# Kernel tuning notes

Hardware: AMD Instinct MI355X
Metric: run time of the kernel (lower is better)

The kernel has to match this reference:

```python
import jax, jax.numpy as jnp
import numpy as np

D_MODEL = 1024
N_HEADS = 16
D_KEY = 64
EPS = 1e-5


def setup_inputs() -> dict:
    key = jax.random.key(0)
    ks = jax.random.split(key, 12)
    d, h, dk = D_MODEL, N_HEADS, D_KEY
    s = lambda fan_in: 1.0 / np.sqrt(fan_in)
    inp = {
        "X": jax.random.normal(ks[0], (2, 2048, d), dtype=jnp.float32),
        "Wqkv": jax.random.uniform(ks[1], (d, 3 * h * dk), jnp.float32, -s(d), s(d)),
        "bqkv": jax.random.uniform(ks[2], (3 * h * dk,), jnp.float32, -s(d), s(d)),
        "Wo": jax.random.uniform(ks[3], (h * dk, d), jnp.float32, -s(h * dk), s(h * dk)),
        "bo": jax.random.uniform(ks[4], (d,), jnp.float32, -s(h * dk), s(h * dk)),
        "W1": jax.random.uniform(ks[5], (d, 4 * d), jnp.float32, -s(d), s(d)),
        "b1": jax.random.uniform(ks[6], (4 * d,), jnp.float32, -s(d), s(d)),
        "W2": jax.random.uniform(ks[7], (4 * d, d), jnp.float32, -s(4 * d), s(4 * d)),
        "b2": jax.random.uniform(ks[8], (d,), jnp.float32, -s(4 * d), s(4 * d)),
        "ln1_g": jnp.ones((d,), jnp.float32),
        "ln1_b": jnp.zeros((d,), jnp.float32),
        "ln2_g": jnp.ones((d,), jnp.float32),
        "ln2_b": jnp.zeros((d,), jnp.float32),
    }
    return inp


def _layernorm(x, g, b):
    mu = jnp.mean(x, axis=-1, keepdims=True)
    var = jnp.var(x, axis=-1, keepdims=True)
    return (x - mu) * jax.lax.rsqrt(var + EPS) * g + b


def _block(X, Wqkv, bqkv, Wo, bo, W1, b1, W2, b2, ln1_g, ln1_b, ln2_g, ln2_b):
    B, T, _ = X.shape
    h, dk = N_HEADS, D_KEY
    # --- causal multi-head self-attention on LN(X) ---
    Xn = _layernorm(X, ln1_g, ln1_b)
    qkv = (Xn @ Wqkv + bqkv).reshape(B, T, 3, h, dk)
    q, k, v = (jnp.moveaxis(qkv, 2, 0)[i].transpose(0, 2, 1, 3) for i in range(3))  # each [B,h,T,dk]
    scores = jnp.einsum("bhqd,bhkd->bhqk", q, k) / np.sqrt(dk).astype(np.float32)
    causal = jnp.tril(jnp.ones((T, T), dtype=bool))
    scores = jnp.where(causal, scores, -jnp.inf)
    attn = jax.nn.softmax(scores, axis=-1)
    ctx = jnp.einsum("bhqk,bhkd->bhqd", attn, v)  # [B,h,T,dk]
    ctx = ctx.transpose(0, 2, 1, 3).reshape(B, T, h * dk)
    atten = ctx @ Wo + bo
    X = X + atten  # dropout is identity in eval mode
    # --- FFN on LN(X) ---
    Xn2 = _layernorm(X, ln2_g, ln2_b)
    ffn = jax.nn.relu(Xn2 @ W1 + b1) @ W2 + b2
    return X + ffn


def reference(X, Wqkv, bqkv, Wo, bo, W1, b1, W2, b2, ln1_g, ln1_b, ln2_g, ln2_b):
    return _block(X, Wqkv, bqkv, Wo, bo, W1, b1, W2, b2, ln1_g, ln1_b, ln2_g, ln2_b)
```

## Files before the change

kernel.cpp:

```cpp
#include <hip/hip_runtime.h>
#include <hip/hip_bf16.h>

typedef __hip_bfloat16 bf16;
typedef __attribute__((ext_vector_type(8))) short short8;
typedef __attribute__((ext_vector_type(4))) float f32x4;

constexpr int D     = 1024;
constexpr int T     = 2048;
constexpr int BATCH = 2;
constexpr int ROWS  = BATCH * T;
constexpr int NH    = 16;
constexpr int DKEY  = 64;
constexpr int QKVN  = 3 * D;
constexpr int FFNN  = 4 * D;

static __device__ __forceinline__ float b2f(bf16 x) { return __bfloat162float(x); }
static __device__ __forceinline__ bf16  f2b(float x) { return __float2bfloat16(x); }
static __device__ __forceinline__ float loadf(const bf16* p)  { return __bfloat162float(*p); }
static __device__ __forceinline__ float loadf(const float* p) { return *p; }
static __device__ __forceinline__ float fast_exp2(float x) { return __builtin_amdgcn_exp2f(x); }
static __device__ __forceinline__ unsigned short f2bu(float x) {
    return __bfloat16_as_ushort(__float2bfloat16(x));
}

__global__ __launch_bounds__(256) void transpose_cast(const float* __restrict__ in,
                                                      bf16* __restrict__ out,
                                                      int R, int C)
{
    __shared__ float tile[32][33];
    int c0 = blockIdx.x * 32, r0 = blockIdx.y * 32;
    int tx = threadIdx.x & 31, ty = threadIdx.x >> 5;
#pragma unroll
    for (int i = 0; i < 32; i += 8)
        tile[ty + i][tx] = in[(size_t)(r0 + ty + i) * C + c0 + tx];
    __syncthreads();
#pragma unroll
    for (int i = 0; i < 32; i += 8)
        out[(size_t)(c0 + ty + i) * R + r0 + tx] = f2b(tile[tx][ty + i]);
}

template <typename TIN>
__global__ __launch_bounds__(256) void ln_kernel(const TIN* __restrict__ X,
                                                 const float* __restrict__ g,
                                                 const float* __restrict__ b,
                                                 bf16* __restrict__ out)
{
    int row = blockIdx.x;
    int tid = threadIdx.x;
    const TIN* xr = X + (size_t)row * D;
    float v[4];
#pragma unroll
    for (int i = 0; i < 4; ++i) v[i] = loadf(xr + tid + i * 256);

    float s1 = v[0] + v[1] + v[2] + v[3];
    float s2 = v[0]*v[0] + v[1]*v[1] + v[2]*v[2] + v[3]*v[3];
#pragma unroll
    for (int off = 32; off; off >>= 1) {
        s1 += __shfl_xor(s1, off);
        s2 += __shfl_xor(s2, off);
    }
    __shared__ float red[8];
    int lane = tid & 63, w = tid >> 6;
    if (lane == 0) { red[w] = s1; red[4 + w] = s2; }
    __syncthreads();
    s1 = red[0] + red[1] + red[2] + red[3];
    s2 = red[4] + red[5] + red[6] + red[7];

    float mu   = s1 * (1.0f / D);
    float var  = s2 * (1.0f / D) - mu * mu;
    float rstd = rsqrtf(var + 1e-5f);

    bf16* orow = out + (size_t)row * D;
#pragma unroll
    for (int i = 0; i < 4; ++i) {
        int c = tid + i * 256;
        orow[c] = f2b((v[i] - mu) * rstd * g[c] + b[c]);
    }
}

template <int BM, int RELU, int RES, int OUTF32>
__global__ __launch_bounds__(256) void mfma_gemm(
    const bf16* __restrict__ A, const bf16* __restrict__ Bt,
    const float* __restrict__ bias, const void* __restrict__ resid,
    void* __restrict__ out, int M, int N, int K)
{
    constexpr int LDSK = 40;
    constexpr int MT   = BM / 32;
    __shared__ __align__(16) unsigned short As[2][BM * LDSK];
    __shared__ __align__(16) unsigned short Bs[2][128 * LDSK];

    int tid  = threadIdx.x;
    int m0   = blockIdx.y * BM, n0 = blockIdx.x * 128;
    int lane = tid & 63, wave = tid >> 6;
    int wm = (wave >> 1) * (MT * 16), wn = (wave & 1) * 64;
    int c15 = lane & 15, quad = lane >> 4;

    f32x4 acc[MT][4] = {};

    int brow = tid >> 1, bseg = (tid & 1) * 16;
    int arow, aseg;
    if constexpr (BM == 128) { arow = tid >> 1; aseg = (tid & 1) * 16; }
    else                     { arow = tid >> 2; aseg = (tid & 3) * 8;  }
    const bf16* aptr = A  + (size_t)(m0 + arow) * K + aseg;
    const bf16* bptr = Bt + (size_t)(n0 + brow) * K + bseg;

    int nk = K >> 5;
    uint4 ra0, ra1, rb0, rb1;
    ra0 = *(const uint4*)(aptr);
    if constexpr (BM == 128) ra1 = *(const uint4*)(aptr + 8);
    rb0 = *(const uint4*)(bptr);
    rb1 = *(const uint4*)(bptr + 8);

    for (int kt = 0; kt < nk; ++kt) {
        int buf = kt & 1;
        {
            unsigned short* asl = &As[buf][arow * LDSK + aseg];
            unsigned short* bsl = &Bs[buf][brow * LDSK + bseg];
            *(uint4*)asl = ra0;
            if constexpr (BM == 128) *(uint4*)(asl + 8) = ra1;
            *(uint4*)bsl       = rb0;
            *(uint4*)(bsl + 8) = rb1;
        }
        __syncthreads();
        if (kt + 1 < nk) {
            int ko = (kt + 1) * 32;
            ra0 = *(const uint4*)(aptr + ko);
            if constexpr (BM == 128) ra1 = *(const uint4*)(aptr + ko + 8);
            rb0 = *(const uint4*)(bptr + ko);
            rb1 = *(const uint4*)(bptr + ko + 8);
        }
        short8 af[MT], bfr[4];
#pragma unroll
        for (int t = 0; t < MT; ++t)
            af[t]  = *(const short8*)&As[buf][(wm + t * 16 + c15) * LDSK + quad * 8];
#pragma unroll
        for (int t = 0; t < 4; ++t)
            bfr[t] = *(const short8*)&Bs[buf][(wn + t * 16 + c15) * LDSK + quad * 8];
#pragma unroll
        for (int mt = 0; mt < MT; ++mt)
#pragma unroll
            for (int nt = 0; nt < 4; ++nt)
                acc[mt][nt] = __builtin_amdgcn_mfma_f32_16x16x32_bf16(
                    af[mt], bfr[nt], acc[mt][nt], 0, 0, 0);
    }

#pragma unroll
    for (int mt = 0; mt < MT; ++mt) {
#pragma unroll
        for (int nt = 0; nt < 4; ++nt) {
            f32x4 v4 = acc[mt][nt];
            int gc = n0 + wn + nt * 16 + c15;
            float bb = bias[gc];
#pragma unroll
            for (int r = 0; r < 4; ++r) {
                int gr = m0 + wm + mt * 16 + quad * 4 + r;
                float v = v4[r] + bb;
                if constexpr (RELU) v = fmaxf(v, 0.0f);
                size_t idx = (size_t)gr * N + gc;
                if constexpr (RES == 1) v += b2f(((const bf16*)resid)[idx]);
                if constexpr (RES == 2) v += ((const float*)resid)[idx];
                if constexpr (OUTF32) ((float*)out)[idx] = v;
                else                  ((bf16*)out)[idx] = f2b(v);
            }
        }
    }
}

__global__ __launch_bounds__(256) void flash_attn(const bf16* __restrict__ qkv,
                                                  bf16* __restrict__ ctx)
{
    constexpr int KROW = 72;
    constexpr float CSC = 0.18033688011112042f;
    constexpr float MSH = 12.0f;

    __shared__ __align__(16) unsigned short Qs[128 * KROW];
    __shared__ __align__(16) unsigned short Ks[64 * KROW];
    __shared__ __align__(16) unsigned short Vt[64 * KROW];
    unsigned short* Pt = Qs;

    int bx = blockIdx.x;
    int bh = bx & 31;
    int qi = 15 - (bx >> 5);
    int h  = bh & 15, b = bh >> 4;
    int q0 = qi * 128;

    int tid = threadIdx.x, lane = tid & 63, w = tid >> 6;
    int c15 = lane & 15, quad = lane >> 4;

    const bf16* base = qkv + (size_t)b * T * QKVN;

    {
        int row = tid >> 1, half = tid & 1;
        const bf16* src = base + (size_t)(q0 + row) * QKVN + h * 64 + half * 32;
        unsigned short* dst = &Qs[row * KROW + half * 32];
        uint4 v0 = *(const uint4*)(src);
        uint4 v1 = *(const uint4*)(src + 8);
        uint4 v2 = *(const uint4*)(src + 16);
        uint4 v3 = *(const uint4*)(src + 24);
        *(uint4*)(dst)      = v0;
        *(uint4*)(dst + 8)  = v1;
        *(uint4*)(dst + 16) = v2;
        *(uint4*)(dst + 24) = v3;
    }
    __syncthreads();

    short8 qf[2][2];
#pragma unroll
    for (int qt = 0; qt < 2; ++qt)
#pragma unroll
        for (int s = 0; s < 2; ++s)
            qf[qt][s] = *(const short8*)&Qs[(w * 32 + qt * 16 + c15) * KROW + s * 32 + quad * 8];

    short8 ones;
#pragma unroll
    for (int i = 0; i < 8; ++i) ones[i] = (short)0x3F80;

    f32x4 Ot[4][2] = {};
    f32x4 lacc[2]  = {};

    int nkt   = q0 / 64 + 2;
    int wqmin = q0 + w * 32;
    int wqmax = wqmin + 31;

    for (int kt = 0; kt < nkt; ++kt) {
        int k0 = kt * 64;
        int key = tid >> 2, seg = tid & 3;
        const bf16* ksrc = base + (size_t)(k0 + key) * QKVN + D + h * 64 + seg * 16;
        uint4 kv0 = *(const uint4*)ksrc;
        uint4 kv1 = *(const uint4*)(ksrc + 8);
        int keyp = (tid & 31) * 2, dk0 = (tid >> 5) * 8;
        const bf16* vsrc = base + (size_t)(k0 + keyp) * QKVN + 2 * D + h * 64 + dk0;
        uint4 vv0 = *(const uint4*)vsrc;
        uint4 vv1 = *(const uint4*)(vsrc + QKVN);

        __syncthreads();
        {
            unsigned short* kd = &Ks[key * KROW + seg * 16];
            *(uint4*)kd       = kv0;
            *(uint4*)(kd + 8) = kv1;
            const unsigned short* lo = (const unsigned short*)&vv0;
            const unsigned short* hi = (const unsigned short*)&vv1;
#pragma unroll
            for (int j = 0; j < 8; ++j) {
                unsigned int pk = (unsigned int)lo[j] | ((unsigned int)hi[j] << 16);
                *(unsigned int*)&Vt[(dk0 + j) * KROW + keyp] = pk;
            }
        }
        __syncthreads();

        if (k0 <= wqmax) {
            f32x4 St[4][2] = {};
#pragma unroll
            for (int s = 0; s < 2; ++s)
#pragma unroll
                for (int ktm = 0; ktm < 4; ++ktm) {
                    short8 kf = *(const short8*)&Ks[(ktm * 16 + c15) * KROW + s * 32 + quad * 8];
#pragma unroll
                    for (int qt = 0; qt < 2; ++qt)
                        St[ktm][qt] = __builtin_amdgcn_mfma_f32_16x16x32_bf16(
                            kf, qf[qt][s], St[ktm][qt], 0, 0, 0);
                }

            bool diag = (k0 + 63 > wqmin);
#pragma unroll
            for (int ktm = 0; ktm < 4; ++ktm)
#pragma unroll
                for (int qt = 0; qt < 2; ++qt) {
                    ushort4 pk;
                    int q_g = wqmin + qt * 16 + c15;
#pragma unroll
                    for (int r = 0; r < 4; ++r) {
                        float p = fast_exp2(fmaf(St[ktm][qt][r], CSC, -MSH));
                        if (diag && (k0 + ktm * 16 + quad * 4 + r > q_g)) p = 0.0f;
                        ((unsigned short*)&pk)[r] = f2bu(p);
                    }
                    *(ushort4*)&Pt[(w * 32 + qt * 16 + c15) * KROW + ktm * 16 + quad * 4] = pk;
                }

#pragma unroll
            for (int s = 0; s < 2; ++s) {
                short8 pf[2];
#pragma unroll
                for (int qt = 0; qt < 2; ++qt)
                    pf[qt] = *(const short8*)&Pt[(w * 32 + qt * 16 + c15) * KROW + s * 32 + quad * 8];
#pragma unroll
                for (int qt = 0; qt < 2; ++qt)
                    lacc[qt] = __builtin_amdgcn_mfma_f32_16x16x32_bf16(ones, pf[qt], lacc[qt], 0, 0, 0);
#pragma unroll
                for (int dt = 0; dt < 4; ++dt) {
                    short8 vf = *(const short8*)&Vt[(dt * 16 + c15) * KROW + s * 32 + quad * 8];
#pragma unroll
                    for (int qt = 0; qt < 2; ++qt)
                        Ot[dt][qt] = __builtin_amdgcn_mfma_f32_16x16x32_bf16(
                            vf, pf[qt], Ot[dt][qt], 0, 0, 0);
                }
            }
        }
    }

#pragma unroll
    for (int qt = 0; qt < 2; ++qt) {
        float inv = 1.0f / lacc[qt][0];
        int grow = b * T + q0 + w * 32 + qt * 16 + c15;
        bf16* dst = ctx + (size_t)grow * D + h * 64 + quad * 4;
#pragma unroll
        for (int dt = 0; dt < 4; ++dt) {
            ushort4 pk;
#pragma unroll
            for (int r = 0; r < 4; ++r)
                ((unsigned short*)&pk)[r] = f2bu(Ot[dt][qt][r] * inv);
            *(ushort4*)(dst + dt * 16) = pk;
        }
    }
}

extern "C" void kernel_launch(void* const* d_in, const int* in_sizes, int n_in,
                              void* d_out, int out_size, void* d_ws, size_t ws_size,
                              hipStream_t stream)
{
    const float* X    = (const float*)d_in[0];
    const float* Wqkv = (const float*)d_in[1];
    const float* bqkv = (const float*)d_in[2];
    const float* Wo   = (const float*)d_in[3];
    const float* bo   = (const float*)d_in[4];
    const float* W1   = (const float*)d_in[5];
    const float* b1   = (const float*)d_in[6];
    const float* W2   = (const float*)d_in[7];
    const float* b2   = (const float*)d_in[8];
    const float* ln1g = (const float*)d_in[9];
    const float* ln1b = (const float*)d_in[10];
    const float* ln2g = (const float*)d_in[11];
    const float* ln2b = (const float*)d_in[12];
    float* out = (float*)d_out;

    char* ws = (char*)d_ws;
    bf16* Wqkv_t = (bf16*)(ws + 0);
    bf16* Wo_t   = (bf16*)(ws + 6291456);
    bf16* W1_t   = (bf16*)(ws + 8388608);
    bf16* W2_t   = (bf16*)(ws + 16777216);
    bf16* Xn     = (bf16*)(ws + 25165824);
    bf16* X1     = Xn;
    bf16* qkv    = (bf16*)(ws + 33554432);
    bf16* Xn2    = (bf16*)(ws + 33554432);
    bf16* ctx    = (bf16*)(ws + 58720256);
    bf16* mid    = (bf16*)(ws + 41943040);

    transpose_cast<<<dim3(QKVN / 32, D / 32), 256, 0, stream>>>(Wqkv, Wqkv_t, D, QKVN);
    transpose_cast<<<dim3(D / 32, D / 32), 256, 0, stream>>>(Wo, Wo_t, D, D);
    transpose_cast<<<dim3(FFNN / 32, D / 32), 256, 0, stream>>>(W1, W1_t, D, FFNN);
    transpose_cast<<<dim3(D / 32, FFNN / 32), 256, 0, stream>>>(W2, W2_t, FFNN, D);

    ln_kernel<float><<<ROWS, 256, 0, stream>>>(X, ln1g, ln1b, Xn);
    mfma_gemm<128, 0, 0, 0><<<dim3(QKVN / 128, ROWS / 128), 256, 0, stream>>>(
        Xn, Wqkv_t, bqkv, nullptr, qkv, ROWS, QKVN, D);
    flash_attn<<<512, 256, 0, stream>>>(qkv, ctx);
    mfma_gemm<64, 0, 2, 0><<<dim3(D / 128, ROWS / 64), 256, 0, stream>>>(
        ctx, Wo_t, bo, X, X1, ROWS, D, D);
    ln_kernel<bf16><<<ROWS, 256, 0, stream>>>(X1, ln2g, ln2b, Xn2);
    mfma_gemm<128, 1, 0, 0><<<dim3(FFNN / 128, ROWS / 128), 256, 0, stream>>>(
        Xn2, W1_t, b1, nullptr, mid, ROWS, FFNN, D);
    mfma_gemm<64, 0, 1, 1><<<dim3(D / 128, ROWS / 64), 256, 0, stream>>>(
        mid, W2_t, b2, X1, out, ROWS, D, FFNN);
}
```

Baseline: 374.7 us.

## Split-K the W2 GEMM into two partials and swizzle workgroup order for XCDs

The final FFN down-projection GEMM is split along K into two halves run as separate grid z-slices. Slice zero writes bias plus residual into the output and slice one writes an fp32 partial into reused workspace. A new elementwise kernel then adds the partial into the output. All GEMMs also remap block IDs so consecutive blocks spread across the 8 XCDs. The goal is more workgroups for the small-N GEMM at the cost of an extra 16MB fp32 partial write, its read back, and one more launch.

```diff
diff --git a/kernel.cpp b/kernel.cpp
--- a/kernel.cpp
+++ b/kernel.cpp
@@ -78,22 +78,35 @@
     }
 }
 
-template <int BM, int RELU, int RES, int OUTF32>
+template <int BM, int RELU, int RES, int OUTF32, int SPLITZ = 0>
 __global__ __launch_bounds__(256) void mfma_gemm(
     const bf16* __restrict__ A, const bf16* __restrict__ Bt,
     const float* __restrict__ bias, const void* __restrict__ resid,
-    void* __restrict__ out, int M, int N, int K)
+    void* __restrict__ out, float* __restrict__ part,
+    int M, int N, int K, int Kstride)
 {
     constexpr int LDSK = 40;
     constexpr int MT   = BM / 32;
     __shared__ __align__(16) unsigned short As[2][BM * LDSK];
     __shared__ __align__(16) unsigned short Bs[2][128 * LDSK];
 
+    int gx = gridDim.x, gy = gridDim.y;
+    int lid = (blockIdx.z * gy + blockIdx.y) * gx + blockIdx.x;
+    int nwg = gx * gy * gridDim.z;
+    int chunk = nwg >> 3;
+    int swz = (lid & 7) * chunk + (lid >> 3);
+    int bx = swz % gx;
+    int by = (swz / gx) % gy;
+    int bz = swz / (gx * gy);
+
     int tid  = threadIdx.x;
-    int m0   = blockIdx.y * BM, n0 = blockIdx.x * 128;
+    int m0   = by * BM, n0 = bx * 128;
     int lane = tid & 63, wave = tid >> 6;
     int wm = (wave >> 1) * (MT * 16), wn = (wave & 1) * 64;
     int c15 = lane & 15, quad = lane >> 4;
+
+    int koff = 0;
+    if constexpr (SPLITZ) koff = bz * K;
 
     f32x4 acc[MT][4] = {};
 
@@ -101,8 +114,8 @@
     int arow, aseg;
     if constexpr (BM == 128) { arow = tid >> 1; aseg = (tid & 1) * 16; }
     else                     { arow = tid >> 2; aseg = (tid & 3) * 8;  }
-    const bf16* aptr = A  + (size_t)(m0 + arow) * K + aseg;
-    const bf16* bptr = Bt + (size_t)(n0 + brow) * K + bseg;
+    const bf16* aptr = A  + (size_t)(m0 + arow) * Kstride + koff + aseg;
+    const bf16* bptr = Bt + (size_t)(n0 + brow) * Kstride + koff + bseg;
 
     int nk = K >> 5;
     uint4 ra0, ra1, rb0, rb1;
@@ -150,20 +163,39 @@
         for (int nt = 0; nt < 4; ++nt) {
             f32x4 v4 = acc[mt][nt];
             int gc = n0 + wn + nt * 16 + c15;
-            float bb = bias[gc];
+            float bb = (!SPLITZ || bz == 0) ? bias[gc] : 0.0f;
 #pragma unroll
             for (int r = 0; r < 4; ++r) {
                 int gr = m0 + wm + mt * 16 + quad * 4 + r;
                 float v = v4[r] + bb;
                 if constexpr (RELU) v = fmaxf(v, 0.0f);
                 size_t idx = (size_t)gr * N + gc;
-                if constexpr (RES == 1) v += b2f(((const bf16*)resid)[idx]);
-                if constexpr (RES == 2) v += ((const float*)resid)[idx];
-                if constexpr (OUTF32) ((float*)out)[idx] = v;
-                else                  ((bf16*)out)[idx] = f2b(v);
+                if constexpr (SPLITZ) {
+                    if (bz == 0) {
+                        v += b2f(((const bf16*)resid)[idx]);
+                        ((float*)out)[idx] = v;
+                    } else {
+                        part[idx] = v;
+                    }
+                } else {
+                    if constexpr (RES == 1) v += b2f(((const bf16*)resid)[idx]);
+                    if constexpr (RES == 2) v += ((const float*)resid)[idx];
+                    if constexpr (OUTF32) ((float*)out)[idx] = v;
+                    else                  ((bf16*)out)[idx] = f2b(v);
+                }
             }
         }
     }
+}
+
+__global__ __launch_bounds__(256) void add_partial(float* __restrict__ out,
+                                                   const float* __restrict__ part)
+{
+    int i = blockIdx.x * 256 + threadIdx.x;
+    f32x4 a = ((const f32x4*)out)[i];
+    f32x4 p = ((const f32x4*)part)[i];
+    a += p;
+    ((f32x4*)out)[i] = a;
 }
 
 __global__ __launch_bounds__(256) void flash_attn(const bf16* __restrict__ qkv,
@@ -344,6 +376,7 @@
     bf16* Xn2    = (bf16*)(ws + 33554432);
     bf16* ctx    = (bf16*)(ws + 58720256);
     bf16* mid    = (bf16*)(ws + 41943040);
+    float* W2part = (float*)(ws + 0);
 
     transpose_cast<<<dim3(QKVN / 32, D / 32), 256, 0, stream>>>(Wqkv, Wqkv_t, D, QKVN);
     transpose_cast<<<dim3(D / 32, D / 32), 256, 0, stream>>>(Wo, Wo_t, D, D);
@@ -352,13 +385,14 @@
 
     ln_kernel<float><<<ROWS, 256, 0, stream>>>(X, ln1g, ln1b, Xn);
     mfma_gemm<128, 0, 0, 0><<<dim3(QKVN / 128, ROWS / 128), 256, 0, stream>>>(
-        Xn, Wqkv_t, bqkv, nullptr, qkv, ROWS, QKVN, D);
+        Xn, Wqkv_t, bqkv, nullptr, qkv, nullptr, ROWS, QKVN, D, D);
     flash_attn<<<512, 256, 0, stream>>>(qkv, ctx);
     mfma_gemm<64, 0, 2, 0><<<dim3(D / 128, ROWS / 64), 256, 0, stream>>>(
-        ctx, Wo_t, bo, X, X1, ROWS, D, D);
+        ctx, Wo_t, bo, X, X1, nullptr, ROWS, D, D, D);
     ln_kernel<bf16><<<ROWS, 256, 0, stream>>>(X1, ln2g, ln2b, Xn2);
     mfma_gemm<128, 1, 0, 0><<<dim3(FFNN / 128, ROWS / 128), 256, 0, stream>>>(
-        Xn2, W1_t, b1, nullptr, mid, ROWS, FFNN, D);
-    mfma_gemm<64, 0, 1, 1><<<dim3(D / 128, ROWS / 64), 256, 0, stream>>>(
-        mid, W2_t, b2, X1, out, ROWS, D, FFNN);
-}
+        Xn2, W1_t, b1, nullptr, mid, nullptr, ROWS, FFNN, D, D);
+    mfma_gemm<64, 0, 1, 1, 1><<<dim3(D / 128, ROWS / 64, 2), 256, 0, stream>>>(
+        mid, W2_t, b2, X1, out, W2part, ROWS, D, FFNN / 2, FFNN);
+    add_partial<<<ROWS * D / 4 / 256, 256, 0, stream>>>(out, W2part);
+}
```

Result: no change. 372.0 us (-0.7%).
